# Kernel tuning notes

Hardware: AMD Instinct MI355X
Metric: run time of the kernel (lower is better)

Reference implementation:

```python
import jax, jax.numpy as jnp
import numpy as np

GROUPS = 16
STRIDE = (1, 1)
PADDING = ((1, 1), (1, 1))
DILATION = (1, 1)


def setup_inputs() -> dict:
    key = jax.random.key(0)
    kx, kw, kb = jax.random.split(key, 3)
    N, Cin, H, Wd = 16, 256, 128, 128
    Cout, k = 512, 3
    cin_per_group = Cin // GROUPS  # 16
    x = jax.random.normal(kx, (N, Cin, H, Wd), dtype=jnp.float32)
    # grouped-conv weight: (Cout, Cin/groups, k, k)
    W = jax.random.normal(kw, (Cout, cin_per_group, k, k), dtype=jnp.float32) * 0.05
    b = jax.random.normal(kb, (Cout,), dtype=jnp.float32) * 0.05
    return {"x": x, "W": W, "b": b}


def reference(x, W, b):
    # Single fused grouped conv (equivalent to the 16-way split/conv/cat loop).
    y = jax.lax.conv_general_dilated(
        x, W,
        window_strides=STRIDE,
        padding=PADDING,
        rhs_dilation=DILATION,
        dimension_numbers=("NCHW", "OIHW", "NCHW"),
        feature_group_count=GROUPS,
    )
    return y + b[None, :, None, None]
```

## Files before the change

kernel.cpp:

```cpp
#include <hip/hip_runtime.h>


#define CIN_PG 16
#define COUT_PG 32
#define HH 128
#define WW 128
#define TH 8
#define TW 32
#define XTH (TH + 2)
#define XTW (TW + 2)
#define NPX (XTH * XTW)
#define PLANE (HH * WW)

typedef __attribute__((ext_vector_type(8))) short bf16x8;
typedef __attribute__((ext_vector_type(16))) float f32x16;
typedef __attribute__((ext_vector_type(4))) unsigned int u32x4;

__device__ __forceinline__ unsigned bfpack(float a, float b) {
    unsigned ua = __builtin_bit_cast(unsigned, a);
    unsigned ub = __builtin_bit_cast(unsigned, b);
    return (ua >> 16) | (ub & 0xffff0000u);
}

__global__ __launch_bounds__(256) void prep_weights(
    const float* __restrict__ wgt, unsigned* __restrict__ wks)
{
    int t = blockIdx.x * 256 + threadIdx.x;
    if (t >= 16 * COUT_PG * 9) return;
    int tap = t % 9;
    int co  = (t / 9) % COUT_PG;
    int g   = t / (9 * COUT_PG);
    const float* src = wgt + ((size_t)(g * COUT_PG + co) * CIN_PG * 9) + tap;
    float v[16], lo[16];
#pragma unroll
    for (int ci = 0; ci < 16; ++ci) {
        v[ci] = src[ci * 9];
        unsigned ub = __builtin_bit_cast(unsigned, v[ci]);
        float hf = __builtin_bit_cast(float, ub & 0xffff0000u);
        lo[ci] = v[ci] - hf;
    }
    u32x4 c[4];
#pragma unroll
    for (int j = 0; j < 4; ++j) {
        c[0][j] = bfpack(v[2 * j], v[2 * j + 1]);
        c[1][j] = bfpack(v[8 + 2 * j], v[8 + 2 * j + 1]);
        c[2][j] = bfpack(lo[2 * j], lo[2 * j + 1]);
        c[3][j] = bfpack(lo[8 + 2 * j], lo[8 + 2 * j + 1]);
    }
    unsigned* dst = wks + (size_t)((g * 9 + tap) * COUT_PG + co) * 16;
    unsigned rot = (co >> 1) & 3;
#pragma unroll
    for (int s = 0; s < 4; ++s) {
        unsigned slot = (s + rot) & 3;
        *(u32x4*)(dst + slot * 4) = c[s];
    }
}

__global__ __launch_bounds__(256, 3) void grouped_conv_mfma(
    const float* __restrict__ x, const unsigned* __restrict__ wks,
    const float* __restrict__ bias, float* __restrict__ out)
{
    __shared__ unsigned xs[NPX * 16];
    __shared__ unsigned ws[9 * COUT_PG * 16];
    __shared__ float bs[COUT_PG];

    const int bx = blockIdx.x;
    const int wtile = bx & 3;
    const int htile = (bx >> 2) & 15;
    const int g = (bx >> 6) & 15;
    const int n = bx >> 10;
    const int h0 = htile * TH;
    const int w0 = wtile * TW;
    const int tid = threadIdx.x;
    const int wave = tid >> 6;
    const int lane = tid & 63;

    {
        const u32x4* wsrc = (const u32x4*)(wks + (size_t)g * (9 * COUT_PG * 16));
        for (int i = tid; i < 9 * COUT_PG * 4; i += 256)
            *(u32x4*)&ws[i * 4] = wsrc[i];
    }
    if (tid < COUT_PG) bs[tid] = bias[g * COUT_PG + tid];

    {
        const float* xg = x + (size_t)(n * 256 + g * CIN_PG) * PLANE;
        for (int p = tid; p < NPX; p += 256) {
            int hh2 = p / XTW;
            int ww2 = p - hh2 * XTW;
            int gh = h0 + hh2 - 1;
            int gw = w0 + ww2 - 1;
            float v[16], lo[16];
            if ((unsigned)gh < HH && (unsigned)gw < WW) {
                const float* xp = xg + (size_t)gh * WW + gw;
#pragma unroll
                for (int ci = 0; ci < 16; ++ci) v[ci] = xp[(size_t)ci * PLANE];
            } else {
#pragma unroll
                for (int ci = 0; ci < 16; ++ci) v[ci] = 0.0f;
            }
#pragma unroll
            for (int ci = 0; ci < 16; ++ci) {
                unsigned ub = __builtin_bit_cast(unsigned, v[ci]);
                float hf = __builtin_bit_cast(float, ub & 0xffff0000u);
                lo[ci] = v[ci] - hf;
            }
            u32x4 c0 = {bfpack(v[0], v[1]), bfpack(v[2], v[3]), bfpack(v[4], v[5]), bfpack(v[6], v[7])};
            u32x4 c1 = {bfpack(v[8], v[9]), bfpack(v[10], v[11]), bfpack(v[12], v[13]), bfpack(v[14], v[15])};
            u32x4 c2 = {bfpack(lo[0], lo[1]), bfpack(lo[2], lo[3]), bfpack(lo[4], lo[5]), bfpack(lo[6], lo[7])};
            u32x4 c3 = {bfpack(lo[8], lo[9]), bfpack(lo[10], lo[11]), bfpack(lo[12], lo[13]), bfpack(lo[14], lo[15])};
            unsigned rot = (p >> 1) & 3;
            unsigned base = p * 16;
            *(u32x4*)&xs[base + (((0 + rot) & 3) << 2)] = c0;
            *(u32x4*)&xs[base + (((1 + rot) & 3) << 2)] = c1;
            *(u32x4*)&xs[base + (((2 + rot) & 3) << 2)] = c2;
            *(u32x4*)&xs[base + (((3 + rot) & 3) << 2)] = c3;
        }
    }
    __syncthreads();

    const int half = lane >> 5;
    const int pxl = lane & 31;

    bf16x8 wfh[9], wfl[9];
    {
        const int co = lane & 31;
        unsigned wrot = (co >> 1) & 3;
#pragma unroll
        for (int tap = 0; tap < 9; ++tap) {
            unsigned b = (unsigned)(tap * COUT_PG + co) * 16;
            unsigned sh = ((half + wrot) & 3) << 2;
            wfh[tap] = __builtin_bit_cast(bf16x8, *(const u32x4*)&ws[b + sh]);
            wfl[tap] = __builtin_bit_cast(bf16x8, *(const u32x4*)&ws[b + (sh ^ 8)]);
        }
    }

    f32x16 a0 = {}, a1 = {};
    const int r0 = wave * 2;

#pragma unroll
    for (int kh = 0; kh < 3; ++kh) {
#pragma unroll
        for (int kw = 0; kw < 3; ++kw) {
            const int tap = kh * 3 + kw;
            int p0 = (r0 + kh) * XTW + pxl + kw;
            int p1 = p0 + XTW;
            unsigned ah0 = (unsigned)p0 * 16 + (((half + ((p0 >> 1) & 3)) & 3) << 2);
            unsigned ah1 = (unsigned)p1 * 16 + (((half + ((p1 >> 1) & 3)) & 3) << 2);
            bf16x8 xh0 = __builtin_bit_cast(bf16x8, *(const u32x4*)&xs[ah0]);
            bf16x8 xl0 = __builtin_bit_cast(bf16x8, *(const u32x4*)&xs[ah0 ^ 8]);
            bf16x8 xh1 = __builtin_bit_cast(bf16x8, *(const u32x4*)&xs[ah1]);
            bf16x8 xl1 = __builtin_bit_cast(bf16x8, *(const u32x4*)&xs[ah1 ^ 8]);
            a0 = __builtin_amdgcn_mfma_f32_32x32x16_bf16(wfh[tap], xh0, a0, 0, 0, 0);
            a1 = __builtin_amdgcn_mfma_f32_32x32x16_bf16(wfh[tap], xh1, a1, 0, 0, 0);
            a0 = __builtin_amdgcn_mfma_f32_32x32x16_bf16(wfh[tap], xl0, a0, 0, 0, 0);
            a1 = __builtin_amdgcn_mfma_f32_32x32x16_bf16(wfh[tap], xl1, a1, 0, 0, 0);
            a0 = __builtin_amdgcn_mfma_f32_32x32x16_bf16(wfl[tap], xh0, a0, 0, 0, 0);
            a1 = __builtin_amdgcn_mfma_f32_32x32x16_bf16(wfl[tap], xh1, a1, 0, 0, 0);
        }
    }

    float* obase = out + (size_t)(n * 512 + g * COUT_PG) * PLANE + (size_t)(h0 + r0) * WW + (w0 + pxl);
#pragma unroll
    for (int r = 0; r < 16; ++r) {
        int cor = (r & 3) + 8 * (r >> 2) + 4 * half;
        obase[(size_t)cor * PLANE] = a0[r] + bs[cor];
    }
    obase += WW;
#pragma unroll
    for (int r = 0; r < 16; ++r) {
        int cor = (r & 3) + 8 * (r >> 2) + 4 * half;
        obase[(size_t)cor * PLANE] = a1[r] + bs[cor];
    }
}

extern "C" void kernel_launch(void* const* d_in, const int* in_sizes, int n_in,
                              void* d_out, int out_size, void* d_ws, size_t ws_size,
                              hipStream_t stream) {
    const float* x = (const float*)d_in[0];
    const float* w = (const float*)d_in[1];
    const float* b = (const float*)d_in[2];
    float* out = (float*)d_out;
    unsigned* wks = (unsigned*)d_ws;
    hipLaunchKernelGGL(prep_weights, dim3(18), dim3(256), 0, stream, w, wks);
    hipLaunchKernelGGL(grouped_conv_mfma, dim3(16384), dim3(256), 0, stream, x, wks, b, out);
}
```

Measured before the change: 732.5 us.

## Make conv kernel persistent with double-buffered input tiles and register-resident weights

Replaces the one-tile-per-block grid with a persistent grid of 768 blocks (48 tile slots per group), where each block loops over tiles of a single group. Weights are loaded once per block from a new MFMA-friendly global layout directly into registers instead of through shared memory. The next tile's input is prefetched into a second shared buffer while the current tile's MFMAs run, and row loads are shared between the two output rows. This aims to hide global load latency and cut repeated weight staging, at the cost of higher register pressure and fewer blocks, which may underfill the GPU or limit occupancy.

```diff
diff --git a/kernel.cpp b/kernel.cpp
--- a/kernel.cpp
+++ b/kernel.cpp
@@ -7,10 +7,12 @@
 #define WW 128
 #define TH 8
 #define TW 32
-#define XTH (TH + 2)
-#define XTW (TW + 2)
-#define NPX (XTH * XTW)
-#define PLANE (HH * WW)
+#define XTH 10
+#define XTW 34
+#define NPX 340
+#define PLANE 16384
+#define NTILES 1024
+#define NSLOTS 48
 
 typedef __attribute__((ext_vector_type(8))) short bf16x8;
 typedef __attribute__((ext_vector_type(16))) float f32x16;
@@ -39,137 +41,181 @@
         float hf = __builtin_bit_cast(float, ub & 0xffff0000u);
         lo[ci] = v[ci] - hf;
     }
-    u32x4 c[4];
+    u32x4 c0, c1, c2, c3;
 #pragma unroll
     for (int j = 0; j < 4; ++j) {
-        c[0][j] = bfpack(v[2 * j], v[2 * j + 1]);
-        c[1][j] = bfpack(v[8 + 2 * j], v[8 + 2 * j + 1]);
-        c[2][j] = bfpack(lo[2 * j], lo[2 * j + 1]);
-        c[3][j] = bfpack(lo[8 + 2 * j], lo[8 + 2 * j + 1]);
-    }
-    unsigned* dst = wks + (size_t)((g * 9 + tap) * COUT_PG + co) * 16;
-    unsigned rot = (co >> 1) & 3;
-#pragma unroll
-    for (int s = 0; s < 4; ++s) {
-        unsigned slot = (s + rot) & 3;
-        *(u32x4*)(dst + slot * 4) = c[s];
-    }
+        c0[j] = bfpack(v[2 * j], v[2 * j + 1]);
+        c1[j] = bfpack(v[8 + 2 * j], v[9 + 2 * j]);
+        c2[j] = bfpack(lo[2 * j], lo[2 * j + 1]);
+        c3[j] = bfpack(lo[8 + 2 * j], lo[9 + 2 * j]);
+    }
+    unsigned* dst = wks + (size_t)(g * 9 + tap) * 512;
+    *(u32x4*)(dst + co * 4)       = c0;
+    *(u32x4*)(dst + 128 + co * 4) = c1;
+    *(u32x4*)(dst + 256 + co * 4) = c2;
+    *(u32x4*)(dst + 384 + co * 4) = c3;
+}
+
+__device__ __forceinline__ void stage_load(const float* __restrict__ xg,
+                                           int h0, int w0, int p, float v[16])
+{
+    int hh = p / XTW;
+    int ww = p - hh * XTW;
+    int gh = h0 + hh - 1;
+    int gw = w0 + ww - 1;
+    if ((unsigned)gh < HH && (unsigned)gw < WW) {
+        const float* xp = xg + (size_t)gh * WW + gw;
+#pragma unroll
+        for (int ci = 0; ci < 16; ++ci) v[ci] = xp[ci * PLANE];
+    } else {
+#pragma unroll
+        for (int ci = 0; ci < 16; ++ci) v[ci] = 0.0f;
+    }
+}
+
+__device__ __forceinline__ void stage_write(unsigned* __restrict__ xbuf,
+                                            int p, const float v[16])
+{
+    float lo[16];
+#pragma unroll
+    for (int ci = 0; ci < 16; ++ci) {
+        unsigned ub = __builtin_bit_cast(unsigned, v[ci]);
+        float hf = __builtin_bit_cast(float, ub & 0xffff0000u);
+        lo[ci] = v[ci] - hf;
+    }
+    u32x4 c0 = {bfpack(v[0], v[1]), bfpack(v[2], v[3]), bfpack(v[4], v[5]), bfpack(v[6], v[7])};
+    u32x4 c1 = {bfpack(v[8], v[9]), bfpack(v[10], v[11]), bfpack(v[12], v[13]), bfpack(v[14], v[15])};
+    u32x4 c2 = {bfpack(lo[0], lo[1]), bfpack(lo[2], lo[3]), bfpack(lo[4], lo[5]), bfpack(lo[6], lo[7])};
+    u32x4 c3 = {bfpack(lo[8], lo[9]), bfpack(lo[10], lo[11]), bfpack(lo[12], lo[13]), bfpack(lo[14], lo[15])};
+    unsigned rot = (p >> 1) & 3;
+    unsigned base = (unsigned)p * 16;
+    *(u32x4*)&xbuf[base + (((0 + rot) & 3) << 2)] = c0;
+    *(u32x4*)&xbuf[base + (((1 + rot) & 3) << 2)] = c1;
+    *(u32x4*)&xbuf[base + (((2 + rot) & 3) << 2)] = c2;
+    *(u32x4*)&xbuf[base + (((3 + rot) & 3) << 2)] = c3;
 }
 
 __global__ __launch_bounds__(256, 3) void grouped_conv_mfma(
     const float* __restrict__ x, const unsigned* __restrict__ wks,
     const float* __restrict__ bias, float* __restrict__ out)
 {
-    __shared__ unsigned xs[NPX * 16];
-    __shared__ unsigned ws[9 * COUT_PG * 16];
+    __shared__ unsigned xs[2][NPX * 16];
     __shared__ float bs[COUT_PG];
 
     const int bx = blockIdx.x;
-    const int wtile = bx & 3;
-    const int htile = (bx >> 2) & 15;
-    const int g = (bx >> 6) & 15;
-    const int n = bx >> 10;
-    const int h0 = htile * TH;
-    const int w0 = wtile * TW;
+    const int g = bx & 15;
+    const int slot = bx >> 4;
     const int tid = threadIdx.x;
     const int wave = tid >> 6;
     const int lane = tid & 63;
-
-    {
-        const u32x4* wsrc = (const u32x4*)(wks + (size_t)g * (9 * COUT_PG * 16));
-        for (int i = tid; i < 9 * COUT_PG * 4; i += 256)
-            *(u32x4*)&ws[i * 4] = wsrc[i];
-    }
-    if (tid < COUT_PG) bs[tid] = bias[g * COUT_PG + tid];
-
-    {
-        const float* xg = x + (size_t)(n * 256 + g * CIN_PG) * PLANE;
-        for (int p = tid; p < NPX; p += 256) {
-            int hh2 = p / XTW;
-            int ww2 = p - hh2 * XTW;
-            int gh = h0 + hh2 - 1;
-            int gw = w0 + ww2 - 1;
-            float v[16], lo[16];
-            if ((unsigned)gh < HH && (unsigned)gw < WW) {
-                const float* xp = xg + (size_t)gh * WW + gw;
-#pragma unroll
-                for (int ci = 0; ci < 16; ++ci) v[ci] = xp[(size_t)ci * PLANE];
-            } else {
-#pragma unroll
-                for (int ci = 0; ci < 16; ++ci) v[ci] = 0.0f;
-            }
-#pragma unroll
-            for (int ci = 0; ci < 16; ++ci) {
-                unsigned ub = __builtin_bit_cast(unsigned, v[ci]);
-                float hf = __builtin_bit_cast(float, ub & 0xffff0000u);
-                lo[ci] = v[ci] - hf;
-            }
-            u32x4 c0 = {bfpack(v[0], v[1]), bfpack(v[2], v[3]), bfpack(v[4], v[5]), bfpack(v[6], v[7])};
-            u32x4 c1 = {bfpack(v[8], v[9]), bfpack(v[10], v[11]), bfpack(v[12], v[13]), bfpack(v[14], v[15])};
-            u32x4 c2 = {bfpack(lo[0], lo[1]), bfpack(lo[2], lo[3]), bfpack(lo[4], lo[5]), bfpack(lo[6], lo[7])};
-            u32x4 c3 = {bfpack(lo[8], lo[9]), bfpack(lo[10], lo[11]), bfpack(lo[12], lo[13]), bfpack(lo[14], lo[15])};
-            unsigned rot = (p >> 1) & 3;
-            unsigned base = p * 16;
-            *(u32x4*)&xs[base + (((0 + rot) & 3) << 2)] = c0;
-            *(u32x4*)&xs[base + (((1 + rot) & 3) << 2)] = c1;
-            *(u32x4*)&xs[base + (((2 + rot) & 3) << 2)] = c2;
-            *(u32x4*)&xs[base + (((3 + rot) & 3) << 2)] = c3;
-        }
-    }
-    __syncthreads();
-
     const int half = lane >> 5;
     const int pxl = lane & 31;
 
+    if (tid < COUT_PG) bs[tid] = bias[g * COUT_PG + tid];
+
     bf16x8 wfh[9], wfl[9];
     {
-        const int co = lane & 31;
-        unsigned wrot = (co >> 1) & 3;
+        const unsigned* wg = wks + (size_t)g * (9 * 512);
 #pragma unroll
         for (int tap = 0; tap < 9; ++tap) {
-            unsigned b = (unsigned)(tap * COUT_PG + co) * 16;
-            unsigned sh = ((half + wrot) & 3) << 2;
-            wfh[tap] = __builtin_bit_cast(bf16x8, *(const u32x4*)&ws[b + sh]);
-            wfl[tap] = __builtin_bit_cast(bf16x8, *(const u32x4*)&ws[b + (sh ^ 8)]);
-        }
-    }
-
-    f32x16 a0 = {}, a1 = {};
-    const int r0 = wave * 2;
-
-#pragma unroll
-    for (int kh = 0; kh < 3; ++kh) {
-#pragma unroll
-        for (int kw = 0; kw < 3; ++kw) {
-            const int tap = kh * 3 + kw;
-            int p0 = (r0 + kh) * XTW + pxl + kw;
-            int p1 = p0 + XTW;
-            unsigned ah0 = (unsigned)p0 * 16 + (((half + ((p0 >> 1) & 3)) & 3) << 2);
-            unsigned ah1 = (unsigned)p1 * 16 + (((half + ((p1 >> 1) & 3)) & 3) << 2);
-            bf16x8 xh0 = __builtin_bit_cast(bf16x8, *(const u32x4*)&xs[ah0]);
-            bf16x8 xl0 = __builtin_bit_cast(bf16x8, *(const u32x4*)&xs[ah0 ^ 8]);
-            bf16x8 xh1 = __builtin_bit_cast(bf16x8, *(const u32x4*)&xs[ah1]);
-            bf16x8 xl1 = __builtin_bit_cast(bf16x8, *(const u32x4*)&xs[ah1 ^ 8]);
-            a0 = __builtin_amdgcn_mfma_f32_32x32x16_bf16(wfh[tap], xh0, a0, 0, 0, 0);
-            a1 = __builtin_amdgcn_mfma_f32_32x32x16_bf16(wfh[tap], xh1, a1, 0, 0, 0);
-            a0 = __builtin_amdgcn_mfma_f32_32x32x16_bf16(wfh[tap], xl0, a0, 0, 0, 0);
-            a1 = __builtin_amdgcn_mfma_f32_32x32x16_bf16(wfh[tap], xl1, a1, 0, 0, 0);
-            a0 = __builtin_amdgcn_mfma_f32_32x32x16_bf16(wfl[tap], xh0, a0, 0, 0, 0);
-            a1 = __builtin_amdgcn_mfma_f32_32x32x16_bf16(wfl[tap], xh1, a1, 0, 0, 0);
-        }
-    }
-
-    float* obase = out + (size_t)(n * 512 + g * COUT_PG) * PLANE + (size_t)(h0 + r0) * WW + (w0 + pxl);
-#pragma unroll
-    for (int r = 0; r < 16; ++r) {
-        int cor = (r & 3) + 8 * (r >> 2) + 4 * half;
-        obase[(size_t)cor * PLANE] = a0[r] + bs[cor];
-    }
-    obase += WW;
-#pragma unroll
-    for (int r = 0; r < 16; ++r) {
-        int cor = (r & 3) + 8 * (r >> 2) + 4 * half;
-        obase[(size_t)cor * PLANE] = a1[r] + bs[cor];
+            const unsigned* tb = wg + tap * 512;
+            wfh[tap] = __builtin_bit_cast(bf16x8, *(const u32x4*)(tb + lane * 4));
+            wfl[tap] = __builtin_bit_cast(bf16x8, *(const u32x4*)(tb + 256 + lane * 4));
+        }
+    }
+
+    {
+        const int t = slot;
+        const int n = t >> 6;
+        const int h0 = ((t >> 2) & 15) * TH;
+        const int w0 = (t & 3) * TW;
+        const float* xg = x + (size_t)(n * 256 + g * CIN_PG) * PLANE;
+        float v[16];
+        stage_load(xg, h0, w0, tid, v);
+        stage_write(xs[0], tid, v);
+        if (tid < NPX - 256) {
+            stage_load(xg, h0, w0, tid + 256, v);
+            stage_write(xs[0], tid + 256, v);
+        }
+    }
+
+    int cur = 0;
+    for (int t = slot; t < NTILES; t += NSLOTS) {
+        __syncthreads();
+
+        const int n = t >> 6;
+        const int h0 = ((t >> 2) & 15) * TH;
+        const int w0 = (t & 3) * TW;
+
+        const bool hasnext = (t + NSLOTS) < NTILES;
+        const float* nxg = x;
+        int nh0 = 0, nw0 = 0;
+        float v1[16];
+        if (hasnext) {
+            const int t2 = t + NSLOTS;
+            nh0 = ((t2 >> 2) & 15) * TH;
+            nw0 = (t2 & 3) * TW;
+            nxg = x + (size_t)((t2 >> 6) * 256 + g * CIN_PG) * PLANE;
+            stage_load(nxg, nh0, nw0, tid, v1);
+        }
+
+        const unsigned* xb = xs[cur];
+        f32x16 a0 = {}, a1 = {};
+        const int r0 = wave * 2;
+
+#pragma unroll
+        for (int r = 0; r < 4; ++r) {
+            bf16x8 xh[3], xl[3];
+#pragma unroll
+            for (int kw = 0; kw < 3; ++kw) {
+                int p = (r0 + r) * XTW + pxl + kw;
+                unsigned a = (unsigned)p * 16 + (((half + ((p >> 1) & 3)) & 3) << 2);
+                xh[kw] = __builtin_bit_cast(bf16x8, *(const u32x4*)&xb[a]);
+                xl[kw] = __builtin_bit_cast(bf16x8, *(const u32x4*)&xb[a ^ 8]);
+            }
+            if (r < 3) {
+#pragma unroll
+                for (int kw = 0; kw < 3; ++kw) {
+                    const int tap = r * 3 + kw;
+                    a0 = __builtin_amdgcn_mfma_f32_32x32x16_bf16(wfh[tap], xh[kw], a0, 0, 0, 0);
+                    a0 = __builtin_amdgcn_mfma_f32_32x32x16_bf16(wfh[tap], xl[kw], a0, 0, 0, 0);
+                    a0 = __builtin_amdgcn_mfma_f32_32x32x16_bf16(wfl[tap], xh[kw], a0, 0, 0, 0);
+                }
+            }
+            if (r > 0) {
+#pragma unroll
+                for (int kw = 0; kw < 3; ++kw) {
+                    const int tap = (r - 1) * 3 + kw;
+                    a1 = __builtin_amdgcn_mfma_f32_32x32x16_bf16(wfh[tap], xh[kw], a1, 0, 0, 0);
+                    a1 = __builtin_amdgcn_mfma_f32_32x32x16_bf16(wfh[tap], xl[kw], a1, 0, 0, 0);
+                    a1 = __builtin_amdgcn_mfma_f32_32x32x16_bf16(wfl[tap], xh[kw], a1, 0, 0, 0);
+                }
+            }
+            if (r == 1 && hasnext) {
+                stage_write(xs[cur ^ 1], tid, v1);
+                if (tid < NPX - 256)
+                    stage_load(nxg, nh0, nw0, tid + 256, v1);
+            }
+        }
+
+        float* ob = out + (size_t)(n * 512 + g * COUT_PG) * PLANE
+                  + (size_t)(h0 + r0) * WW + (w0 + pxl);
+#pragma unroll
+        for (int rr = 0; rr < 16; ++rr) {
+            int cor = (rr & 3) + 8 * (rr >> 2) + 4 * half;
+            ob[(size_t)cor * PLANE] = a0[rr] + bs[cor];
+        }
+        ob += WW;
+#pragma unroll
+        for (int rr = 0; rr < 16; ++rr) {
+            int cor = (rr & 3) + 8 * (rr >> 2) + 4 * half;
+            ob[(size_t)cor * PLANE] = a1[rr] + bs[cor];
+        }
+
+        if (hasnext && tid < NPX - 256)
+            stage_write(xs[cur ^ 1], tid + 256, v1);
+
+        cur ^= 1;
     }
 }
 
@@ -182,5 +228,6 @@
     float* out = (float*)d_out;
     unsigned* wks = (unsigned*)d_ws;
     hipLaunchKernelGGL(prep_weights, dim3(18), dim3(256), 0, stream, w, wks);
-    hipLaunchKernelGGL(grouped_conv_mfma, dim3(16384), dim3(256), 0, stream, x, wks, b, out);
-}
+    hipLaunchKernelGGL(grouped_conv_mfma, dim3(768), dim3(256), 0, stream,
+                       x, wks, b, out);
+}
```

New measurement: 892.1 us. 1.22x slower.
